# Performance work log

Hardware: AMD Instinct MI355X
Metric: run time of the kernel (lower is better)

## Reference

```python
import jax, jax.numpy as jnp
import numpy as np

N = 50000   # nodes
E = 800000  # edges
G = 128     # graphs in batch
IN_DIM = 5
HID = 64
EPS = 1e-5


def setup_inputs() -> dict:
    key = jax.random.key(0)
    ks = jax.random.split(key, 8)
    x = jax.random.normal(ks[0], (N, IN_DIM), dtype=jnp.float32)
    edge_index = jax.random.randint(ks[1], (2, E), 0, N, dtype=jnp.int64)
    edge_weight = jax.random.uniform(ks[2], (E,), dtype=jnp.float32)
    batch = jnp.sort(jax.random.randint(ks[3], (N,), 0, G, dtype=jnp.int64))
    W1 = jax.random.normal(ks[4], (IN_DIM, HID), dtype=jnp.float32) * (1.0 / np.sqrt(IN_DIM))
    W2 = jax.random.normal(ks[5], (HID, HID), dtype=jnp.float32) * (1.0 / np.sqrt(HID))
    lin1_W = jax.random.normal(ks[6], (HID, HID // 2), dtype=jnp.float32) * (1.0 / np.sqrt(HID))
    lin2_W = jax.random.normal(ks[7], (HID // 2, 1), dtype=jnp.float32) * (1.0 / np.sqrt(HID // 2))
    return {
        "x": x, "edge_index": edge_index, "edge_weight": edge_weight, "batch": batch,
        "W1": W1, "b1": jnp.zeros((HID,), jnp.float32),
        "W2": W2, "b2": jnp.zeros((HID,), jnp.float32),
        "bn1_gamma": jnp.ones((HID,), jnp.float32), "bn1_beta": jnp.zeros((HID,), jnp.float32),
        "bn1_mean": jnp.zeros((HID,), jnp.float32), "bn1_var": jnp.ones((HID,), jnp.float32),
        "bn2_gamma": jnp.ones((HID,), jnp.float32), "bn2_beta": jnp.zeros((HID,), jnp.float32),
        "bn2_mean": jnp.zeros((HID,), jnp.float32), "bn2_var": jnp.ones((HID,), jnp.float32),
        "lin1_W": lin1_W, "lin1_b": jnp.zeros((HID // 2,), jnp.float32),
        "lin2_W": lin2_W, "lin2_b": jnp.zeros((1,), jnp.float32),
    }


def gcn_conv(x, edge_index, edge_weight, W, b):
    # PyG GCNConv: add self-loops (weight 1), symmetric normalization, scatter-add at dst.
    src, dst = edge_index[0], edge_index[1]
    loop = jnp.arange(N, dtype=src.dtype)
    s = jnp.concatenate([src, loop])
    d = jnp.concatenate([dst, loop])
    w = jnp.concatenate([edge_weight, jnp.ones((N,), edge_weight.dtype)])
    deg = jax.ops.segment_sum(w, d, num_segments=N)  # [N]
    dinv = jnp.where(deg > 0, jax.lax.rsqrt(jnp.maximum(deg, 1e-12)), 0.0)
    norm = dinv[s] * w * dinv[d]                      # [E+N]
    h = x @ W                                         # project first (small GEMM)
    msg = norm[:, None] * h[s]                        # [E+N, H] gather
    return jax.ops.segment_sum(msg, d, num_segments=N) + b


def batchnorm_eval(x, gamma, beta, mean, var):
    return (x - mean) * jax.lax.rsqrt(var + EPS) * gamma + beta


def reference(x, edge_index, edge_weight, batch,
              W1, b1, W2, b2,
              bn1_gamma, bn1_beta, bn1_mean, bn1_var,
              bn2_gamma, bn2_beta, bn2_mean, bn2_var,
              lin1_W, lin1_b, lin2_W, lin2_b):
    h = gcn_conv(x, edge_index, edge_weight, W1, b1)
    h = jax.nn.relu(batchnorm_eval(h, bn1_gamma, bn1_beta, bn1_mean, bn1_var))
    h = gcn_conv(h, edge_index, edge_weight, W2, b2)
    h = jax.nn.relu(batchnorm_eval(h, bn2_gamma, bn2_beta, bn2_mean, bn2_var))
    # global mean pool over graphs
    sums = jax.ops.segment_sum(h, batch, num_segments=G)                 # [G, H]
    cnt = jax.ops.segment_sum(jnp.ones((N,), h.dtype), batch, num_segments=G)
    pooled = sums / jnp.maximum(cnt, 1.0)[:, None]
    z = jax.nn.relu(pooled @ lin1_W + lin1_b)
    out = z @ lin2_W + lin2_b                                            # [G, 1]
    return out.squeeze(-1)
```

## Files before the change

kernel.cpp:

```cpp
#include <hip/hip_runtime.h>
#include <hip/hip_fp16.h>

#define NN 50000
#define NE 800000
#define NG 128
#define IND 5
#define HID 64
#define EPSV 1e-5f

#define NB 391
#define PH_T 1024
#define PH_E 16384
#define PH_WG ((NE + PH_E - 1) / PH_E)

__global__ void k_part_hist(const int* __restrict__ dst, int* __restrict__ h_wg,
                            float* __restrict__ pool_zero) {
    __shared__ int h[NB];
    int tid = threadIdx.x;
    int zgid = blockIdx.x * PH_T + tid;
    if (zgid < NG * HID + NG) pool_zero[zgid] = 0.f;
    for (int j = tid; j < NB; j += PH_T) h[j] = 0;
    __syncthreads();
    int base = blockIdx.x * PH_E;
    for (int k = 0; k < PH_E; k += PH_T) {
        int e = base + k + tid;
        if (e < NE) atomicAdd(&h[dst[e] >> 7], 1);
    }
    __syncthreads();
    for (int j = tid; j < NB; j += PH_T) h_wg[blockIdx.x * NB + j] = h[j];
}

__global__ void k_bscan(const int* __restrict__ h_wg, int* __restrict__ wgbase,
                        int* __restrict__ beb) {
    __shared__ int sm[512];
    int t = threadIdx.x;
    int tot = 0;
    if (t < NB) {
        for (int w = 0; w < PH_WG; w++) {
            wgbase[w * NB + t] = tot;
            tot += h_wg[w * NB + t];
        }
    }
    sm[t] = (t < NB) ? tot : 0;
    __syncthreads();
    for (int off = 1; off < 512; off <<= 1) {
        int v = (t >= off) ? sm[t - off] : 0;
        __syncthreads();
        sm[t] += v;
        __syncthreads();
    }
    if (t <= NB) beb[t] = t ? sm[t - 1] : 0;
    if (t < NB) {
        int base = t ? sm[t - 1] : 0;
        for (int w = 0; w < PH_WG; w++) wgbase[w * NB + t] += base;
    }
}

__global__ void k_part_scatter(const int* __restrict__ src, const int* __restrict__ dst,
                               const float* __restrict__ ew, const int* __restrict__ wgbase,
                               int4* __restrict__ stage) {
    __shared__ int cur[NB];
    __shared__ int base[NB];
    int tid = threadIdx.x;
    int w = blockIdx.x;
    for (int j = tid; j < NB; j += PH_T) { cur[j] = 0; base[j] = wgbase[w * NB + j]; }
    __syncthreads();
    int eb = w * PH_E;
    for (int k = 0; k < PH_E; k += PH_T) {
        int e = eb + k + tid;
        if (e < NE) {
            int d = dst[e], b = d >> 7;
            int off = atomicAdd(&cur[b], 1);
            stage[base[b] + off] = make_int4(src[e], __float_as_int(ew[e]), d, 0);
        }
    }
}

__global__ void k_bucket_fill(const int4* __restrict__ stage, const int* __restrict__ beb,
                              const float* __restrict__ x,
                              int* __restrict__ row_ptr, int2* __restrict__ csr,
                              float* __restrict__ dinv, float* __restrict__ px) {
    __shared__ int cnt[128];
    __shared__ float deg[128];
    __shared__ int cur[128];
    __shared__ int sc[128];
    int b = blockIdx.x, tid = threadIdx.x;
    if (tid < 128) { cnt[tid] = 0; deg[tid] = 0.f; cur[tid] = 0; }
    __syncthreads();
    int eb0 = beb[b], eb1 = beb[b + 1];
    for (int i = eb0 + tid; i < eb1; i += 256) {
        int4 t = stage[i];
        int j = t.z & 127;
        atomicAdd(&cnt[j], 1);
        atomicAdd(&deg[j], __int_as_float(t.y));
    }
    __syncthreads();
    if (tid < 128) sc[tid] = cnt[tid];
    __syncthreads();
    for (int off = 1; off < 128; off <<= 1) {
        int v = 0;
        if (tid < 128 && tid >= off) v = sc[tid - off];
        __syncthreads();
        if (tid < 128) sc[tid] += v;
        __syncthreads();
    }
    if (tid < 128) {
        int n = b * 128 + tid;
        int ex = tid ? sc[tid - 1] : 0;
        if (n <= NN) row_ptr[n] = eb0 + ex;
        if (n < NN) {
            float di = rsqrtf(deg[tid] + 1.0f);
            dinv[n] = di;
            float4 a, bb;
            a.x = di * x[n * IND + 0]; a.y = di * x[n * IND + 1];
            a.z = di * x[n * IND + 2]; a.w = di * x[n * IND + 3];
            bb.x = di * x[n * IND + 4]; bb.y = 0.f; bb.z = 0.f; bb.w = 0.f;
            ((float4*)px)[n * 2 + 0] = a;
            ((float4*)px)[n * 2 + 1] = bb;
        }
    }
    __syncthreads();
    for (int i = eb0 + tid; i < eb1; i += 256) {
        int4 t = stage[i];
        int j = t.z & 127;
        int ex = j ? sc[j - 1] : 0;
        int off = atomicAdd(&cur[j], 1);
        csr[eb0 + ex + off] = make_int2(t.x, t.y);
    }
}

__global__ void k_gather_x(const float* __restrict__ px, const float* __restrict__ dinv,
                           const int* __restrict__ row_ptr, const int2* __restrict__ csr,
                           float* __restrict__ xa) {
    int gid = blockIdx.x * blockDim.x + threadIdx.x;
    if (gid >= NN * 16) return;
    int n = gid >> 4, lane16 = gid & 15;
    const float4* p4 = (const float4*)px;
    int beg = row_ptr[n], end = row_ptr[n + 1];
    float4 a0 = make_float4(0.f, 0.f, 0.f, 0.f);
    float a4 = 0.f;
    int i = beg + lane16;
    if (i < end) {
        long long cur = __builtin_nontemporal_load((const long long*)&csr[i]);
        for (; i < end; i += 16) {
            int pi = (i + 16 < end) ? i + 16 : i;
            long long nxt = __builtin_nontemporal_load((const long long*)&csr[pi]);
            int   s = (int)(cur & 0xffffffffLL);
            float w = __int_as_float((int)(cur >> 32));
            float4 v0 = p4[s * 2 + 0];
            float  v4 = px[s * 8 + 4];
            a0.x += w * v0.x; a0.y += w * v0.y; a0.z += w * v0.z; a0.w += w * v0.w;
            a4 += w * v4;
            cur = nxt;
        }
    }
#pragma unroll
    for (int m = 8; m >= 1; m >>= 1) {
        a0.x += __shfl_xor(a0.x, m); a0.y += __shfl_xor(a0.y, m);
        a0.z += __shfl_xor(a0.z, m); a0.w += __shfl_xor(a0.w, m);
        a4 += __shfl_xor(a4, m);
    }
    if (lane16 == 0) {
        float di = dinv[n];
        float4 v0 = p4[n * 2 + 0];
        float  v4 = px[n * 8 + 4];
        float4 o0;
        o0.x = di * (a0.x + v0.x); o0.y = di * (a0.y + v0.y);
        o0.z = di * (a0.z + v0.z); o0.w = di * (a0.w + v0.w);
        ((float4*)xa)[n * 2 + 0] = o0;
        ((float4*)xa)[n * 2 + 1] = make_float4(di * (a4 + v4), 0.f, 0.f, 0.f);
    }
}

__global__ void k_gemm1_fused(const float* __restrict__ xa, const float* __restrict__ W1,
                              const float* __restrict__ b1,
                              const float* __restrict__ gamma, const float* __restrict__ beta,
                              const float* __restrict__ mean, const float* __restrict__ var,
                              float* __restrict__ outv) {
    __shared__ float Ws[IND * HID];
    for (int j = threadIdx.x; j < IND * HID; j += blockDim.x) Ws[j] = W1[j];
    __syncthreads();
    int gid = blockIdx.x * blockDim.x + threadIdx.x;
    if (gid >= NN * HID) return;
    int n = gid >> 6, hc = gid & 63;
    const float* xr = &xa[n * 8];
    float acc = b1[hc];
#pragma unroll
    for (int k = 0; k < IND; k++) acc += xr[k] * Ws[k * HID + hc];
    float r = fmaxf((acc - mean[hc]) * rsqrtf(var[hc] + EPSV) * gamma[hc] + beta[hc], 0.f);
    outv[gid] = r;
}

__global__ void k_gemm2_h16(const float* __restrict__ a, const float* __restrict__ W,
                            const float* __restrict__ dinv, __half* __restrict__ tab) {
    __shared__ float4 Ws4[HID * 16];
    {
        const float4* W4 = (const float4*)W;
        for (int j = threadIdx.x; j < HID * 16; j += blockDim.x) Ws4[j] = W4[j];
    }
    __syncthreads();
    int gid = blockIdx.x * blockDim.x + threadIdx.x;
    if (gid >= NN * 16) return;
    int n = gid >> 4, q = gid & 15;
    const float4* ar4 = (const float4*)&a[n * HID];
    float acc0 = 0.f, acc1 = 0.f, acc2 = 0.f, acc3 = 0.f;
#pragma unroll
    for (int k4 = 0; k4 < 16; k4++) {
        float4 av = ar4[k4];
        float4 w0 = Ws4[(k4 * 4 + 0) * 16 + q];
        float4 w1 = Ws4[(k4 * 4 + 1) * 16 + q];
        float4 w2 = Ws4[(k4 * 4 + 2) * 16 + q];
        float4 w3 = Ws4[(k4 * 4 + 3) * 16 + q];
        acc0 += av.x * w0.x + av.y * w1.x + av.z * w2.x + av.w * w3.x;
        acc1 += av.x * w0.y + av.y * w1.y + av.z * w2.y + av.w * w3.y;
        acc2 += av.x * w0.z + av.y * w1.z + av.z * w2.z + av.w * w3.z;
        acc3 += av.x * w0.w + av.y * w1.w + av.z * w2.w + av.w * w3.w;
    }
    float di = dinv[n];
    __half2 h01 = __floats2half2_rn(di * acc0, di * acc1);
    __half2 h23 = __floats2half2_rn(di * acc2, di * acc3);
    uint2 packed;
    packed.x = *(const unsigned int*)&h01;
    packed.y = *(const unsigned int*)&h23;
    ((uint2*)tab)[gid] = packed;
}

__global__ void k_gather_pool(const __half* __restrict__ tab, const float* __restrict__ dinv,
                              const int* __restrict__ row_ptr, const int2* __restrict__ csr,
                              const float* __restrict__ bias,
                              const float* __restrict__ gamma, const float* __restrict__ beta,
                              const float* __restrict__ mean, const float* __restrict__ var,
                              const int* __restrict__ batch,
                              float* pool, float* cnt) {
    __shared__ float lds[16 * HID];
    __shared__ int gs[16];
    int tid = threadIdx.x;
    int gid = blockIdx.x * blockDim.x + tid;
    int n = gid >> 4, c4 = gid & 15;
    int nl = tid >> 4;
    if (tid < 16) gs[tid] = batch[blockIdx.x * 16 + tid];

    const uint2* hq = (const uint2*)tab;
    int beg = row_ptr[n], end = row_ptr[n + 1];

    uint2 sraw = hq[n * 16 + c4];
    float2 s01 = __half22float2(*(const __half2*)&sraw.x);
    float2 s23 = __half22float2(*(const __half2*)&sraw.y);
    float a0 = s01.x, a1 = s01.y, a2 = s23.x, a3 = s23.y;

    if (beg < end) {
        int last = end - 1;
        int i = beg;
        long long c0l = __builtin_nontemporal_load((const long long*)&csr[i]);
        long long c1l = __builtin_nontemporal_load((const long long*)&csr[(i + 1 < end) ? i + 1 : last]);
        long long c2l = __builtin_nontemporal_load((const long long*)&csr[(i + 2 < end) ? i + 2 : last]);
        long long c3l = __builtin_nontemporal_load((const long long*)&csr[(i + 3 < end) ? i + 3 : last]);
        for (; i + 4 <= end; i += 4) {
            long long p0 = __builtin_nontemporal_load((const long long*)&csr[(i + 4 < end) ? i + 4 : last]);
            long long p1 = __builtin_nontemporal_load((const long long*)&csr[(i + 5 < end) ? i + 5 : last]);
            long long p2 = __builtin_nontemporal_load((const long long*)&csr[(i + 6 < end) ? i + 6 : last]);
            long long p3 = __builtin_nontemporal_load((const long long*)&csr[(i + 7 < end) ? i + 7 : last]);
            int   s0 = (int)(c0l & 0xffffffffLL);
            int   s1 = (int)(c1l & 0xffffffffLL);
            int   s2 = (int)(c2l & 0xffffffffLL);
            int   s3 = (int)(c3l & 0xffffffffLL);
            float w0 = __int_as_float((int)(c0l >> 32));
            float w1 = __int_as_float((int)(c1l >> 32));
            float w2 = __int_as_float((int)(c2l >> 32));
            float w3 = __int_as_float((int)(c3l >> 32));
            uint2 r0 = hq[s0 * 16 + c4];
            uint2 r1 = hq[s1 * 16 + c4];
            uint2 r2 = hq[s2 * 16 + c4];
            uint2 r3 = hq[s3 * 16 + c4];
            float2 f;
            f = __half22float2(*(const __half2*)&r0.x); a0 += w0 * f.x; a1 += w0 * f.y;
            f = __half22float2(*(const __half2*)&r0.y); a2 += w0 * f.x; a3 += w0 * f.y;
            f = __half22float2(*(const __half2*)&r1.x); a0 += w1 * f.x; a1 += w1 * f.y;
            f = __half22float2(*(const __half2*)&r1.y); a2 += w1 * f.x; a3 += w1 * f.y;
            f = __half22float2(*(const __half2*)&r2.x); a0 += w2 * f.x; a1 += w2 * f.y;
            f = __half22float2(*(const __half2*)&r2.y); a2 += w2 * f.x; a3 += w2 * f.y;
            f = __half22float2(*(const __half2*)&r3.x); a0 += w3 * f.x; a1 += w3 * f.y;
            f = __half22float2(*(const __half2*)&r3.y); a2 += w3 * f.x; a3 += w3 * f.y;
            c0l = p0; c1l = p1; c2l = p2; c3l = p3;
        }
        int rem = end - i;
        if (rem > 0) {
            int   s0 = (int)(c0l & 0xffffffffLL);
            float w0 = __int_as_float((int)(c0l >> 32));
            uint2 r0 = hq[s0 * 16 + c4];
            float2 f;
            f = __half22float2(*(const __half2*)&r0.x); a0 += w0 * f.x; a1 += w0 * f.y;
            f = __half22float2(*(const __half2*)&r0.y); a2 += w0 * f.x; a3 += w0 * f.y;
        }
        if (rem > 1) {
            int   s1 = (int)(c1l & 0xffffffffLL);
            float w1 = __int_as_float((int)(c1l >> 32));
            uint2 r1 = hq[s1 * 16 + c4];
            float2 f;
            f = __half22float2(*(const __half2*)&r1.x); a0 += w1 * f.x; a1 += w1 * f.y;
            f = __half22float2(*(const __half2*)&r1.y); a2 += w1 * f.x; a3 += w1 * f.y;
        }
        if (rem > 2) {
            int   s2 = (int)(c2l & 0xffffffffLL);
            float w2 = __int_as_float((int)(c2l >> 32));
            uint2 r2 = hq[s2 * 16 + c4];
            float2 f;
            f = __half22float2(*(const __half2*)&r2.x); a0 += w2 * f.x; a1 += w2 * f.y;
            f = __half22float2(*(const __half2*)&r2.y); a2 += w2 * f.x; a3 += w2 * f.y;
        }
    }

    float di = dinv[n];
    int c0 = c4 * 4;
    float4 r;
    {
        float v0 = di * a0 + bias[c0 + 0];
        float v1 = di * a1 + bias[c0 + 1];
        float v2 = di * a2 + bias[c0 + 2];
        float v3 = di * a3 + bias[c0 + 3];
        r.x = fmaxf((v0 - mean[c0 + 0]) * rsqrtf(var[c0 + 0] + EPSV) * gamma[c0 + 0] + beta[c0 + 0], 0.f);
        r.y = fmaxf((v1 - mean[c0 + 1]) * rsqrtf(var[c0 + 1] + EPSV) * gamma[c0 + 1] + beta[c0 + 1], 0.f);
        r.z = fmaxf((v2 - mean[c0 + 2]) * rsqrtf(var[c0 + 2] + EPSV) * gamma[c0 + 2] + beta[c0 + 2], 0.f);
        r.w = fmaxf((v3 - mean[c0 + 3]) * rsqrtf(var[c0 + 3] + EPSV) * gamma[c0 + 3] + beta[c0 + 3], 0.f);
    }
    ((float4*)lds)[nl * 16 + c4] = r;
    __syncthreads();

    if (tid < HID) {
        int c = tid;
        float run = lds[0 * HID + c];
        int gprev = gs[0];
#pragma unroll
        for (int node = 1; node < 16; node++) {
            int g = gs[node];
            float v = lds[node * HID + c];
            if (g != gprev) { atomicAdd(&pool[gprev * HID + c], run); run = v; gprev = g; }
            else run += v;
        }
        atomicAdd(&pool[gprev * HID + c], run);
    } else if (tid == HID) {
        int run = 1, gprev = gs[0];
        for (int node = 1; node < 16; node++) {
            int g = gs[node];
            if (g != gprev) { atomicAdd(&cnt[gprev], (float)run); run = 0; gprev = g; }
            run++;
        }
        atomicAdd(&cnt[gprev], (float)run);
    }
}

__global__ void k_mlp(const float* __restrict__ pool_sums, const float* __restrict__ cnt,
                      const float* __restrict__ l1W, const float* __restrict__ l1b,
                      const float* __restrict__ l2W, const float* __restrict__ l2b,
                      float* __restrict__ outp) {
    int g = blockIdx.x;
    int lane = threadIdx.x;
    int j = lane & 31, kh = lane >> 5;
    const float* pg = &pool_sums[g * HID];
    float z = 0.f;
#pragma unroll 8
    for (int k = kh * 32; k < kh * 32 + 32; k++)
        z += pg[k] * l1W[k * (HID / 2) + j];
    z += __shfl_xor(z, 32);
    float inv = 1.0f / fmaxf(cnt[g], 1.0f);
    float acc = (kh == 0) ? fmaxf(z * inv + l1b[j], 0.f) * l2W[j] : 0.f;
#pragma unroll
    for (int m = 16; m >= 1; m >>= 1) acc += __shfl_xor(acc, m);
    if (lane == 0) outp[g] = acc + l2b[0];
}

extern "C" void kernel_launch(void* const* d_in, const int* in_sizes, int n_in,
                              void* d_out, int out_size, void* d_ws, size_t ws_size,
                              hipStream_t stream) {
    const float* x   = (const float*)d_in[0];
    const int*   ei  = (const int*)d_in[1];
    const float* ew  = (const float*)d_in[2];
    const int*   bat = (const int*)d_in[3];
    const float* W1  = (const float*)d_in[4];
    const float* b1  = (const float*)d_in[5];
    const float* W2  = (const float*)d_in[6];
    const float* b2  = (const float*)d_in[7];
    const float* g1  = (const float*)d_in[8];
    const float* be1 = (const float*)d_in[9];
    const float* m1  = (const float*)d_in[10];
    const float* v1  = (const float*)d_in[11];
    const float* g2  = (const float*)d_in[12];
    const float* be2 = (const float*)d_in[13];
    const float* m2  = (const float*)d_in[14];
    const float* v2  = (const float*)d_in[15];
    const float* l1W = (const float*)d_in[16];
    const float* l1b = (const float*)d_in[17];
    const float* l2W = (const float*)d_in[18];
    const float* l2b = (const float*)d_in[19];
    float* out = (float*)d_out;

    const int* src = ei;
    const int* dst = ei + NE;

    float* f = (float*)d_ws;
    float* pool      = f + 0;
    float* cnt       = f + 8192;
    int*   h_wg      = (int*)(f + 8320);
    int*   wgbase    = (int*)(f + 27479);
    int*   beb       = (int*)(f + 46638);
    int*   row_ptr   = (int*)(f + 47030);
    int2*  csr       = (int2*)(f + 97032);
    float* dinv      = f + 1697032;
    float* px        = f + 1747032;
    float* xa        = f + 2147032;
    float* bufC      = f + 2547032;
    int4*  stage     = (int4*)(f + 2547032);
    __half* tab      = (__half*)(f + 5747032);

    const int BLK = 256;
    const int gNH  = (NN * HID + BLK - 1) / BLK;
    const int gN16 = (NN * 16 + BLK - 1) / BLK;

    k_part_hist<<<PH_WG, PH_T, 0, stream>>>(dst, h_wg, pool);
    k_bscan<<<1, 512, 0, stream>>>(h_wg, wgbase, beb);
    k_part_scatter<<<PH_WG, PH_T, 0, stream>>>(src, dst, ew, wgbase, stage);
    k_bucket_fill<<<NB, BLK, 0, stream>>>(stage, beb, x, row_ptr, csr, dinv, px);

    k_gather_x<<<gN16, BLK, 0, stream>>>(px, dinv, row_ptr, csr, xa);
    k_gemm1_fused<<<gNH, BLK, 0, stream>>>(xa, W1, b1, g1, be1, m1, v1, bufC);

    k_gemm2_h16<<<gN16, BLK, 0, stream>>>(bufC, W2, dinv, tab);
    k_gather_pool<<<gN16, BLK, 0, stream>>>(tab, dinv, row_ptr, csr, b2,
                                            g2, be2, m2, v2, bat, pool, cnt);

    k_mlp<<<NG, 64, 0, stream>>>(pool, cnt, l1W, l1b, l2W, l2b, out);
}
```

Before: 130.8 us.

## Fuse layer-1 projection into layer-2 GEMM and shrink edge staging records

Merges the W1 projection, batchnorm and ReLU kernel into the W2 fp16 projection kernel, keeping the 64-wide hidden row in shared memory so the N x 64 fp32 intermediate is never written to or re-read from global memory. It also replaces the 16-byte int4 staging record in the edge partition with an 8-byte (src, weight) pair plus a 1-byte local destination index, cutting scatter and bucket-fill traffic. The trade-offs are a small byte-array write with poor coalescing and an extra shared-memory barrier in the fused kernel.

```diff
diff --git a/kernel.cpp b/kernel.cpp
--- a/kernel.cpp
+++ b/kernel.cpp
@@ -58,7 +58,7 @@
 
 __global__ void k_part_scatter(const int* __restrict__ src, const int* __restrict__ dst,
                                const float* __restrict__ ew, const int* __restrict__ wgbase,
-                               int4* __restrict__ stage) {
+                               int2* __restrict__ stage_sw, unsigned char* __restrict__ ldst) {
     __shared__ int cur[NB];
     __shared__ int base[NB];
     int tid = threadIdx.x;
@@ -71,13 +71,16 @@
         if (e < NE) {
             int d = dst[e], b = d >> 7;
             int off = atomicAdd(&cur[b], 1);
-            stage[base[b] + off] = make_int4(src[e], __float_as_int(ew[e]), d, 0);
-        }
-    }
-}
-
-__global__ void k_bucket_fill(const int4* __restrict__ stage, const int* __restrict__ beb,
-                              const float* __restrict__ x,
+            int pos = base[b] + off;
+            stage_sw[pos] = make_int2(src[e], __float_as_int(ew[e]));
+            ldst[pos] = (unsigned char)(d & 127);
+        }
+    }
+}
+
+__global__ void k_bucket_fill(const int2* __restrict__ stage_sw,
+                              const unsigned char* __restrict__ ldst,
+                              const int* __restrict__ beb, const float* __restrict__ x,
                               int* __restrict__ row_ptr, int2* __restrict__ csr,
                               float* __restrict__ dinv, float* __restrict__ px) {
     __shared__ int cnt[128];
@@ -89,10 +92,9 @@
     __syncthreads();
     int eb0 = beb[b], eb1 = beb[b + 1];
     for (int i = eb0 + tid; i < eb1; i += 256) {
-        int4 t = stage[i];
-        int j = t.z & 127;
+        int j = ldst[i];
         atomicAdd(&cnt[j], 1);
-        atomicAdd(&deg[j], __int_as_float(t.y));
+        atomicAdd(&deg[j], __int_as_float(stage_sw[i].y));
     }
     __syncthreads();
     if (tid < 128) sc[tid] = cnt[tid];
@@ -121,11 +123,11 @@
     }
     __syncthreads();
     for (int i = eb0 + tid; i < eb1; i += 256) {
-        int4 t = stage[i];
-        int j = t.z & 127;
+        int2 t = stage_sw[i];
+        int j = ldst[i];
         int ex = j ? sc[j - 1] : 0;
         int off = atomicAdd(&cur[j], 1);
-        csr[eb0 + ex + off] = make_int2(t.x, t.y);
+        csr[eb0 + ex + off] = t;
     }
 }
 
@@ -172,41 +174,48 @@
     }
 }
 
-__global__ void k_gemm1_fused(const float* __restrict__ xa, const float* __restrict__ W1,
-                              const float* __restrict__ b1,
-                              const float* __restrict__ gamma, const float* __restrict__ beta,
-                              const float* __restrict__ mean, const float* __restrict__ var,
-                              float* __restrict__ outv) {
-    __shared__ float Ws[IND * HID];
-    for (int j = threadIdx.x; j < IND * HID; j += blockDim.x) Ws[j] = W1[j];
-    __syncthreads();
-    int gid = blockIdx.x * blockDim.x + threadIdx.x;
-    if (gid >= NN * HID) return;
-    int n = gid >> 6, hc = gid & 63;
-    const float* xr = &xa[n * 8];
-    float acc = b1[hc];
-#pragma unroll
-    for (int k = 0; k < IND; k++) acc += xr[k] * Ws[k * HID + hc];
-    float r = fmaxf((acc - mean[hc]) * rsqrtf(var[hc] + EPSV) * gamma[hc] + beta[hc], 0.f);
-    outv[gid] = r;
-}
-
-__global__ void k_gemm2_h16(const float* __restrict__ a, const float* __restrict__ W,
-                            const float* __restrict__ dinv, __half* __restrict__ tab) {
+__global__ void k_proj_fused(const float* __restrict__ xa, const float* __restrict__ W1,
+                             const float* __restrict__ b1,
+                             const float* __restrict__ g1, const float* __restrict__ be1,
+                             const float* __restrict__ m1, const float* __restrict__ v1,
+                             const float* __restrict__ W2, const float* __restrict__ dinv,
+                             __half* __restrict__ tab) {
+    __shared__ float4 W1s4[IND * 16];
     __shared__ float4 Ws4[HID * 16];
+    __shared__ float4 h1s[16 * 16];
     {
-        const float4* W4 = (const float4*)W;
-        for (int j = threadIdx.x; j < HID * 16; j += blockDim.x) Ws4[j] = W4[j];
-    }
-    __syncthreads();
-    int gid = blockIdx.x * blockDim.x + threadIdx.x;
-    if (gid >= NN * 16) return;
-    int n = gid >> 4, q = gid & 15;
-    const float4* ar4 = (const float4*)&a[n * HID];
+        const float4* W14 = (const float4*)W1;
+        for (int j = threadIdx.x; j < IND * 16; j += blockDim.x) W1s4[j] = W14[j];
+        const float4* W24 = (const float4*)W2;
+        for (int j = threadIdx.x; j < HID * 16; j += blockDim.x) Ws4[j] = W24[j];
+    }
+    __syncthreads();
+    int tid = threadIdx.x;
+    int nl = tid >> 4, q = tid & 15;
+    int n = blockIdx.x * 16 + nl;
+    float4 v0 = ((const float4*)xa)[n * 2];
+    float  v4 = xa[n * 8 + 4];
+    int c0 = q * 4;
+    float4 acc;
+    {
+        float4 w0 = W1s4[0 * 16 + q], w1 = W1s4[1 * 16 + q], w2 = W1s4[2 * 16 + q];
+        float4 w3 = W1s4[3 * 16 + q], w4 = W1s4[4 * 16 + q];
+        acc.x = b1[c0 + 0] + v0.x * w0.x + v0.y * w1.x + v0.z * w2.x + v0.w * w3.x + v4 * w4.x;
+        acc.y = b1[c0 + 1] + v0.x * w0.y + v0.y * w1.y + v0.z * w2.y + v0.w * w3.y + v4 * w4.y;
+        acc.z = b1[c0 + 2] + v0.x * w0.z + v0.y * w1.z + v0.z * w2.z + v0.w * w3.z + v4 * w4.z;
+        acc.w = b1[c0 + 3] + v0.x * w0.w + v0.y * w1.w + v0.z * w2.w + v0.w * w3.w + v4 * w4.w;
+    }
+    float4 r;
+    r.x = fmaxf((acc.x - m1[c0 + 0]) * rsqrtf(v1[c0 + 0] + EPSV) * g1[c0 + 0] + be1[c0 + 0], 0.f);
+    r.y = fmaxf((acc.y - m1[c0 + 1]) * rsqrtf(v1[c0 + 1] + EPSV) * g1[c0 + 1] + be1[c0 + 1], 0.f);
+    r.z = fmaxf((acc.z - m1[c0 + 2]) * rsqrtf(v1[c0 + 2] + EPSV) * g1[c0 + 2] + be1[c0 + 2], 0.f);
+    r.w = fmaxf((acc.w - m1[c0 + 3]) * rsqrtf(v1[c0 + 3] + EPSV) * g1[c0 + 3] + be1[c0 + 3], 0.f);
+    h1s[nl * 16 + q] = r;
+    __syncthreads();
     float acc0 = 0.f, acc1 = 0.f, acc2 = 0.f, acc3 = 0.f;
 #pragma unroll
     for (int k4 = 0; k4 < 16; k4++) {
-        float4 av = ar4[k4];
+        float4 av = h1s[nl * 16 + k4];
         float4 w0 = Ws4[(k4 * 4 + 0) * 16 + q];
         float4 w1 = Ws4[(k4 * 4 + 1) * 16 + q];
         float4 w2 = Ws4[(k4 * 4 + 2) * 16 + q];
@@ -222,7 +231,7 @@
     uint2 packed;
     packed.x = *(const unsigned int*)&h01;
     packed.y = *(const unsigned int*)&h23;
-    ((uint2*)tab)[gid] = packed;
+    ((uint2*)tab)[n * 16 + q] = packed;
 }
 
 __global__ void k_gather_pool(const __half* __restrict__ tab, const float* __restrict__ dinv,
@@ -314,14 +323,14 @@
     int c0 = c4 * 4;
     float4 r;
     {
-        float v0 = di * a0 + bias[c0 + 0];
-        float v1 = di * a1 + bias[c0 + 1];
-        float v2 = di * a2 + bias[c0 + 2];
-        float v3 = di * a3 + bias[c0 + 3];
-        r.x = fmaxf((v0 - mean[c0 + 0]) * rsqrtf(var[c0 + 0] + EPSV) * gamma[c0 + 0] + beta[c0 + 0], 0.f);
-        r.y = fmaxf((v1 - mean[c0 + 1]) * rsqrtf(var[c0 + 1] + EPSV) * gamma[c0 + 1] + beta[c0 + 1], 0.f);
-        r.z = fmaxf((v2 - mean[c0 + 2]) * rsqrtf(var[c0 + 2] + EPSV) * gamma[c0 + 2] + beta[c0 + 2], 0.f);
-        r.w = fmaxf((v3 - mean[c0 + 3]) * rsqrtf(var[c0 + 3] + EPSV) * gamma[c0 + 3] + beta[c0 + 3], 0.f);
+        float vv0 = di * a0 + bias[c0 + 0];
+        float vv1 = di * a1 + bias[c0 + 1];
+        float vv2 = di * a2 + bias[c0 + 2];
+        float vv3 = di * a3 + bias[c0 + 3];
+        r.x = fmaxf((vv0 - mean[c0 + 0]) * rsqrtf(var[c0 + 0] + EPSV) * gamma[c0 + 0] + beta[c0 + 0], 0.f);
+        r.y = fmaxf((vv1 - mean[c0 + 1]) * rsqrtf(var[c0 + 1] + EPSV) * gamma[c0 + 1] + beta[c0 + 1], 0.f);
+        r.z = fmaxf((vv2 - mean[c0 + 2]) * rsqrtf(var[c0 + 2] + EPSV) * gamma[c0 + 2] + beta[c0 + 2], 0.f);
+        r.w = fmaxf((vv3 - mean[c0 + 3]) * rsqrtf(var[c0 + 3] + EPSV) * gamma[c0 + 3] + beta[c0 + 3], 0.f);
     }
     ((float4*)lds)[nl * 16 + c4] = r;
     __syncthreads();
@@ -408,23 +417,21 @@
     float* dinv      = f + 1697032;
     float* px        = f + 1747032;
     float* xa        = f + 2147032;
-    float* bufC      = f + 2547032;
-    int4*  stage     = (int4*)(f + 2547032);
-    __half* tab      = (__half*)(f + 5747032);
+    int2*  stage_sw  = (int2*)(f + 2547032);
+    unsigned char* ldst = (unsigned char*)(f + 4147032);
+    __half* tab      = (__half*)(f + 4347032);
 
     const int BLK = 256;
-    const int gNH  = (NN * HID + BLK - 1) / BLK;
     const int gN16 = (NN * 16 + BLK - 1) / BLK;
 
     k_part_hist<<<PH_WG, PH_T, 0, stream>>>(dst, h_wg, pool);
     k_bscan<<<1, 512, 0, stream>>>(h_wg, wgbase, beb);
-    k_part_scatter<<<PH_WG, PH_T, 0, stream>>>(src, dst, ew, wgbase, stage);
-    k_bucket_fill<<<NB, BLK, 0, stream>>>(stage, beb, x, row_ptr, csr, dinv, px);
+    k_part_scatter<<<PH_WG, PH_T, 0, stream>>>(src, dst, ew, wgbase, stage_sw, ldst);
+    k_bucket_fill<<<NB, BLK, 0, stream>>>(stage_sw, ldst, beb, x, row_ptr, csr, dinv, px);
 
     k_gather_x<<<gN16, BLK, 0, stream>>>(px, dinv, row_ptr, csr, xa);
-    k_gemm1_fused<<<gNH, BLK, 0, stream>>>(xa, W1, b1, g1, be1, m1, v1, bufC);
-
-    k_gemm2_h16<<<gN16, BLK, 0, stream>>>(bufC, W2, dinv, tab);
+    k_proj_fused<<<gN16, BLK, 0, stream>>>(xa, W1, b1, g1, be1, m1, v1, W2, dinv, tab);
+
     k_gather_pool<<<gN16, BLK, 0, stream>>>(tab, dinv, row_ptr, csr, b2,
                                             g2, be2, m2, v2, bat, pool, cnt);
 
```

Measured after the change: 133.8 us. 2.3% more time.
